# Kernel optimization log

Measured on AMD Instinct MI355X. Metric: run time of the kernel, lower is better.

## Reference

```python
import jax, jax.numpy as jnp
import numpy as np

B, Nq, Nk, R = 4, 1024, 1024, 256
NH, DK, DV = 8, 64, 64


def setup_inputs() -> dict:
    key = jax.random.key(0)
    ks = jax.random.split(key, 16)
    mk = lambda k, shape, s=1.0: jax.random.normal(k, shape, dtype=jnp.float32) * s
    inp = {
        'Q_real': mk(ks[0], (B, Nq, R)), 'Q_imag': mk(ks[1], (B, Nq, R)),
        'K_real': mk(ks[2], (B, Nk, R)), 'K_imag': mk(ks[3], (B, Nk, R)),
        'V_real': mk(ks[4], (B, Nk, R)), 'V_imag': mk(ks[5], (B, Nk, R)),
        'WQ_r': mk(ks[6], (NH * DK, R), 0.02), 'WQ_i': mk(ks[7], (NH * DK, R), 0.02),
        'WK_r': mk(ks[8], (NH * DK, R), 0.02), 'WK_i': mk(ks[9], (NH * DK, R), 0.02),
        'WV_r': mk(ks[10], (NH * DV, R), 0.02), 'WV_i': mk(ks[11], (NH * DV, R), 0.02),
        'WO_r': mk(ks[12], (R, NH * DV), 0.02), 'WO_i': mk(ks[13], (R, NH * DV), 0.02),
        'mask': jax.random.randint(ks[14], (B, Nk), 0, 2).astype(bool),
    }
    return inp


def _complex_linear(x, w_r, w_i):
    # x: complex [..., in]; weights real [out, in]. Same math as 4 real matmuls.
    w = (w_r + 1j * w_i).astype(jnp.complex64)
    return x @ w.T


def reference(Q_real, Q_imag, K_real, K_imag, V_real, V_imag,
              WQ_r, WQ_i, WK_r, WK_i, WV_r, WV_i, WO_r, WO_i, mask):
    Q = (Q_real + 1j * Q_imag).astype(jnp.complex64)
    K = (K_real + 1j * K_imag).astype(jnp.complex64)
    V = (V_real + 1j * V_imag).astype(jnp.complex64)

    Qp = _complex_linear(Q, WQ_r, WQ_i).reshape(B, Nq, NH, DK).transpose(0, 2, 1, 3)
    Kp = _complex_linear(K, WK_r, WK_i).reshape(B, Nk, NH, DK).transpose(0, 2, 1, 3)
    Vp = _complex_linear(V, WV_r, WV_i).reshape(B, Nk, NH, DV).transpose(0, 2, 1, 3)

    # complex scores [B, NH, Nq, Nk]; conj on K matches torch .conj().transpose
    scores = jnp.einsum('bhqd,bhkd->bhqk', Qp, jnp.conj(Kp)) / jnp.sqrt(jnp.float32(DK))
    scores_abs = jnp.abs(scores)

    m = mask[:, None, None, :]                    # [B,1,1,Nk]
    valid = jnp.any(mask, axis=-1)[:, None, None, None]  # [B,1,1,1] valid query rows
    masked = jnp.where(m, scores_abs, -jnp.inf)
    # avoid all -inf rows feeding softmax (those rows are zeroed afterwards)
    safe = jnp.where(valid, masked, 0.0)
    w = jax.nn.softmax(safe, axis=-1)
    w = jnp.where(valid, w, 0.0)

    attn = jnp.einsum('bhqk,bhkd->bhqd', w.astype(Vp.dtype), Vp)
    attn = attn.transpose(0, 2, 1, 3).reshape(B, Nq, NH * DV)
    return _complex_linear(attn, WO_r, WO_i)
```

## Files before the change

kernel.cpp:

```cpp
#include <hip/hip_runtime.h>
#include <math.h>

#define NBATCH 4
#define NSEQ   1024
#define RD     256
#define NHEAD  8
#define HD     64
#define NHD    512

typedef __attribute__((ext_vector_type(8))) short  short8;
typedef __attribute__((ext_vector_type(4))) short  short4v;
typedef __attribute__((ext_vector_type(4))) float  float4v;

#define MFMA16(a,b,c) __builtin_amdgcn_mfma_f32_16x16x32_bf16(a,b,c,0,0,0)

typedef const void __attribute__((address_space(1)))* gas_t;
typedef void __attribute__((address_space(3)))* las_t;
#define GLOAD16(g, l) __builtin_amdgcn_global_load_lds((gas_t)(g), (las_t)(l), 16, 0, 0)

static __device__ __forceinline__ unsigned short f2b(float f) {
    union { float f; unsigned u; } x; x.f = f;
    unsigned r = x.u + 0x7fffu + ((x.u >> 16) & 1u);
    return (unsigned short)(r >> 16);
}
static __device__ __forceinline__ void st4(short* dst, float4v v) {
    short4v p;
    p[0] = (short)f2b(v[0]); p[1] = (short)f2b(v[1]);
    p[2] = (short)f2b(v[2]); p[3] = (short)f2b(v[3]);
    *(short4v*)dst = p;
}

struct ConvArgs { const float* src[15]; short* dst[15]; int n4[15]; };

__global__ __launch_bounds__(256) void convert_bf16(ConvArgs ca)
{
    const int a = blockIdx.y;
    if (a == 14) {
        if (blockIdx.x != 0) return;
        __shared__ int isByteLayout;
        const int t = threadIdx.x;
        if (t == 0) isByteLayout = 0;
        __syncthreads();
        const int* mi = (const int*)ca.src[14];
        #pragma unroll
        for (int j = 0; j < 4; j++) {
            int v = mi[t*4 + j];
            if (v & ~1) isByteLayout = 1;
        }
        __syncthreads();
        unsigned char* nm = (unsigned char*)ca.dst[14];
        const unsigned char* mb = (const unsigned char*)ca.src[14];
        if (isByteLayout) {
            #pragma unroll
            for (int j = 0; j < 16; j++) { int k = t*16 + j; nm[k] = mb[k] ? 1 : 0; }
        } else {
            #pragma unroll
            for (int j = 0; j < 16; j++) { int k = t*16 + j; nm[k] = mi[k] ? 1 : 0; }
        }
        return;
    }
    const float* __restrict__ s = ca.src[a];
    short* __restrict__ d = ca.dst[a];
    const int n4 = ca.n4[a];
    for (int i = blockIdx.x*256 + threadIdx.x; i < n4; i += gridDim.x*256) {
        float4v v = *(const float4v*)(s + (size_t)i*4);
        st4(d + (size_t)i*4, v);
    }
}

struct ProjArgs {
    const short* Xr[3]; const short* Xi[3];
    const short* Wr[3]; const short* Wi[3];
    short* Yr[3]; short* Yi[3];
};

__global__ __launch_bounds__(256) void cgemm_proj(ProjArgs pa)
{
    __shared__ short sX[2][128][64];
    __shared__ short sW[2][64][64];
    const int z = blockIdx.z;
    const short* __restrict__ X_r = pa.Xr[z];
    const short* __restrict__ X_i = pa.Xi[z];
    const short* __restrict__ W_r = pa.Wr[z];
    const short* __restrict__ W_i = pa.Wi[z];
    short* __restrict__ Y_r = pa.Yr[z];
    short* __restrict__ Y_i = pa.Yi[z];
    const int transposeOut = (z == 2);

    const int tid  = threadIdx.x;
    const int lane = tid & 63, wave = tid >> 6;
    const int quad = lane >> 4, l16 = lane & 15;
    const int sw8  = l16 & 7;
    const int rsub = lane >> 3;
    const int colg = (lane & 7) ^ rsub;
    const int n0 = blockIdx.x * 64, m0 = blockIdx.y * 128;

    const short nk = (short)0x8000;
    const short8 neg = {nk,nk,nk,nk,nk,nk,nk,nk};

    float4v zf = {0.f,0.f,0.f,0.f};
    float4v Yr[2][4], Yi[2][4];
    #pragma unroll
    for (int ms = 0; ms < 2; ms++)
        #pragma unroll
        for (int t = 0; t < 4; t++) { Yr[ms][t] = zf; Yi[ms][t] = zf; }

    for (int kc = 0; kc < RD; kc += 64) {
        __syncthreads();
        if (wave < 2) {
            const short* gp = wave ? X_i : X_r;
            short* lp = wave ? &sX[1][0][0] : &sX[0][0][0];
            #pragma unroll
            for (int j = 0; j < 16; j++) {
                int row = j*8 + rsub;
                GLOAD16(gp + (size_t)(m0 + row)*RD + kc + colg*8, lp + j*512);
            }
        } else {
            const short* gp = (wave == 3) ? W_i : W_r;
            short* lp = (wave == 3) ? &sW[1][0][0] : &sW[0][0][0];
            #pragma unroll
            for (int j = 0; j < 8; j++) {
                int row = j*8 + rsub;
                GLOAD16(gp + (size_t)(n0 + row)*RD + kc + colg*8, lp + j*512);
            }
        }
        __syncthreads();
        short8 fxr[2][2], fxi[2][2], fxin[2][2];
        #pragma unroll
        for (int ms = 0; ms < 2; ms++)
            #pragma unroll
            for (int ds = 0; ds < 2; ds++) {
                int row = wave*32 + ms*16 + l16;
                int u = ((ds*4 + quad) ^ sw8) * 8;
                fxr[ms][ds]  = *(short8*)&sX[0][row][u];
                fxi[ms][ds]  = *(short8*)&sX[1][row][u];
                fxin[ms][ds] = fxi[ms][ds] ^ neg;
            }
        #pragma unroll
        for (int t = 0; t < 4; t++)
            #pragma unroll
            for (int ds = 0; ds < 2; ds++) {
                int u = ((ds*4 + quad) ^ sw8) * 8;
                short8 wr = *(short8*)&sW[0][t*16 + l16][u];
                short8 wi = *(short8*)&sW[1][t*16 + l16][u];
                #pragma unroll
                for (int ms = 0; ms < 2; ms++) {
                    Yr[ms][t] = MFMA16(fxr[ms][ds],  wr, Yr[ms][t]);
                    Yr[ms][t] = MFMA16(fxin[ms][ds], wi, Yr[ms][t]);
                    Yi[ms][t] = MFMA16(fxr[ms][ds],  wi, Yi[ms][t]);
                    Yi[ms][t] = MFMA16(fxi[ms][ds],  wr, Yi[ms][t]);
                }
            }
    }

    const int b = m0 >> 10, h = n0 >> 6, nb = m0 & 1023;
    short* sT = &sX[0][0][0];
    short* Yp[2] = { Y_r, Y_i };
    #pragma unroll
    for (int p = 0; p < 2; p++) {
        __syncthreads();
        #pragma unroll
        for (int ms = 0; ms < 2; ms++)
            #pragma unroll
            for (int t = 0; t < 4; t++)
                #pragma unroll
                for (int r = 0; r < 4; r++) {
                    float v = p ? Yi[ms][t][r] : Yr[ms][t][r];
                    int rr = wave*32 + ms*16 + quad*4 + r;
                    int cc = t*16 + l16;
                    if (!transposeOut) sT[rr*68 + cc]  = (short)f2b(v);
                    else               sT[cc*132 + rr] = (short)f2b(v);
                }
        __syncthreads();
        #pragma unroll
        for (int it = 0; it < 4; it++) {
            int idx = it*256 + tid;
            int rr, c8;
            size_t o;
            const short* sp;
            if (!transposeOut) {
                rr = idx >> 3; c8 = (idx & 7)*8;
                sp = &sT[rr*68 + c8];
                o = (((size_t)(b*NHEAD + h))*NSEQ + nb + rr)*HD + c8;
            } else {
                rr = idx >> 4; c8 = (idx & 15)*8;
                sp = &sT[rr*132 + c8];
                o = (((size_t)(b*NHEAD + h))*HD + rr)*NSEQ + nb + c8;
            }
            short4v a = *(short4v*)sp;
            short4v bq = *(short4v*)(sp + 4);
            short8 v8 = { a[0],a[1],a[2],a[3], bq[0],bq[1],bq[2],bq[3] };
            *(short8*)&Yp[p][o] = v8;
        }
    }
}

__global__ __launch_bounds__(512) void attn_mfma(
    const short* __restrict__ Qp_r, const short* __restrict__ Qp_i,
    const short* __restrict__ Kp_r, const short* __restrict__ Kp_i,
    const short* __restrict__ Vp_r, const short* __restrict__ Vp_i,
    const unsigned char* __restrict__ mask,
    short* __restrict__ Ar, short* __restrict__ Ai)
{
    __shared__ __align__(16) char smem[76800];
    short (*sP)[16][40] = (short(*)[16][40])(smem + 65536);
    unsigned char* smask = (unsigned char*)(smem + 75776);

    const int tid  = threadIdx.x;
    const int lane = tid & 63, wave = tid >> 6;
    const int quad = lane >> 4, l16 = lane & 15;
    const int sw8  = l16 & 7;
    const int qstrip = wave >> 1;
    const int khalf  = wave & 1;
    const int qt = blockIdx.x >> 5;
    const int bh = blockIdx.x & 31;
    const int b  = bh >> 3, h = bh & 7;
    const size_t base = (size_t)bh * (NSEQ*HD);

    const int rsub = lane >> 3;
    const int colg = (lane & 7) ^ rsub;

    if (tid < 256) ((int*)smask)[tid] = ((const int*)(mask + b*NSEQ))[tid];

    const int splane = wave >> 1;
    const short* sgp = (splane == 0) ? Kp_r : (splane == 1) ? Kp_i
                     : (splane == 2) ? Vp_r : Vp_i;
    const int sisV = (splane >= 2);
    const int soff = splane * 8192;

    const short nk = (short)0x8000;
    const short8 neg = {nk,nk,nk,nk,nk,nk,nk,nk};
    short8 fqr[2], fqi[2], fqrn[2];
    #pragma unroll
    for (int ds = 0; ds < 2; ds++) {
        size_t qo = base + (size_t)(qt*64 + qstrip*16 + l16)*HD + ds*32 + quad*8;
        fqr[ds]  = *(const short8*)&Qp_r[qo];
        fqi[ds]  = *(const short8*)&Qp_i[qo];
        fqrn[ds] = fqr[ds] ^ neg;
    }

    float4v zf = {0.f,0.f,0.f,0.f};
    float4v Or[4], Oi[4];
    float lrow[4];
    #pragma unroll
    for (int t = 0; t < 4; t++) { Or[t] = zf; Oi[t] = zf; }
    #pragma unroll
    for (int r = 0; r < 4; r++) lrow[r] = 0.f;

    const float C2 = 0.18033688f;

    {
        short* lp = (short*)(smem + soff);
        #pragma unroll
        for (int jj = 0; jj < 4; jj++) {
            int j = (wave & 1)*4 + jj;
            int row = j*8 + rsub;
            const short* g = sisV
                ? sgp + base + (size_t)row*NSEQ + colg*8
                : sgp + base + (size_t)row*HD + colg*8;
            GLOAD16(g, lp + j*512);
        }
    }

    for (int kt = 0; kt < 16; kt++) {
        __syncthreads();

        if (kt + 1 < 16) {
            const int kn = (kt + 1) * 64;
            short* lp = (short*)(smem + ((kt + 1) & 1)*32768 + soff);
            #pragma unroll
            for (int jj = 0; jj < 4; jj++) {
                int j = (wave & 1)*4 + jj;
                int row = j*8 + rsub;
                const short* g = sisV
                    ? sgp + base + (size_t)row*NSEQ + kn + colg*8
                    : sgp + base + (size_t)(kn + row)*HD + colg*8;
                GLOAD16(g, lp + j*512);
            }
        }

        const char* buf = smem + (kt & 1)*32768;
        short (*sK0)[64] = (short(*)[64])(buf);
        short (*sK1)[64] = (short(*)[64])(buf + 8192);
        short (*sV0)[64] = (short(*)[64])(buf + 16384);
        short (*sV1)[64] = (short(*)[64])(buf + 24576);
        const int k0 = kt*64;

        float4v Sr[2], Si[2];
        Sr[0] = zf; Sr[1] = zf; Si[0] = zf; Si[1] = zf;
        #pragma unroll
        for (int t = 0; t < 2; t++)
            #pragma unroll
            for (int ds = 0; ds < 2; ds++) {
                int u = ((ds*4 + quad) ^ sw8) * 8;
                int krow = khalf*32 + t*16 + l16;
                short8 kr = *(short8*)&sK0[krow][u];
                short8 ki = *(short8*)&sK1[krow][u];
                Sr[t] = MFMA16(fqr[ds],  kr, Sr[t]);
                Sr[t] = MFMA16(fqi[ds],  ki, Sr[t]);
                Si[t] = MFMA16(fqi[ds],  kr, Si[t]);
                Si[t] = MFMA16(fqrn[ds], ki, Si[t]);
            }

        #pragma unroll
        for (int t = 0; t < 2; t++) {
            bool mv = smask[k0 + khalf*32 + t*16 + l16] != 0;
            #pragma unroll
            for (int r = 0; r < 4; r++) {
                float a = Sr[t][r], c = Si[t][r];
                float x = fmaf(a, a, c*c);
                float s = __builtin_amdgcn_sqrtf(x);
                float e = mv ? __builtin_amdgcn_exp2f(C2 * s) : 0.f;
                lrow[r] += e;
                sP[wave][quad*4 + r][t*16 + l16] = (short)f2b(e);
            }
        }

        {
            short8 fp = *(short8*)&sP[wave][l16][quad*8];
            #pragma unroll
            for (int t = 0; t < 4; t++) {
                int u = ((khalf*4 + quad) ^ sw8) * 8;
                short8 vr = *(short8*)&sV0[t*16 + l16][u];
                short8 vi = *(short8*)&sV1[t*16 + l16][u];
                Or[t] = MFMA16(fp, vr, Or[t]);
                Oi[t] = MFMA16(fp, vi, Oi[t]);
            }
        }
    }

    __syncthreads();
    float* sC = (float*)smem;
    float* sL = (float*)(smem + 32768);
    if (khalf == 1) {
        #pragma unroll
        for (int t = 0; t < 4; t++)
            #pragma unroll
            for (int r = 0; r < 4; r++) {
                int o8 = ((qstrip*4 + t)*64 + lane)*8 + r*2;
                sC[o8]     = Or[t][r];
                sC[o8 + 1] = Oi[t][r];
            }
        int lo = (qstrip*64 + lane)*4;
        #pragma unroll
        for (int r = 0; r < 4; r++) sL[lo + r] = lrow[r];
    }
    __syncthreads();
    if (khalf == 0) {
        #pragma unroll
        for (int t = 0; t < 4; t++)
            #pragma unroll
            for (int r = 0; r < 4; r++) {
                int o8 = ((qstrip*4 + t)*64 + lane)*8 + r*2;
                Or[t][r] += sC[o8];
                Oi[t][r] += sC[o8 + 1];
            }
        int lo = (qstrip*64 + lane)*4;
        float inv[4];
        #pragma unroll
        for (int r = 0; r < 4; r++) {
            float ls = lrow[r] + sL[lo + r];
            ls += __shfl_xor(ls, 1, 64);
            ls += __shfl_xor(ls, 2, 64);
            ls += __shfl_xor(ls, 4, 64);
            ls += __shfl_xor(ls, 8, 64);
            inv[r] = (ls > 0.f) ? 1.f/ls : 0.f;
        }
        #pragma unroll
        for (int t = 0; t < 4; t++)
            #pragma unroll
            for (int r = 0; r < 4; r++) {
                int q = qt*64 + qstrip*16 + quad*4 + r;
                int d = t*16 + l16;
                size_t o = ((size_t)(b*NSEQ + q))*NHD + h*HD + d;
                Ar[o] = (short)f2b(Or[t][r] * inv[r]);
                Ai[o] = (short)f2b(Oi[t][r] * inv[r]);
            }
    }
}

__global__ __launch_bounds__(256) void cgemm_out(
    const short* __restrict__ A_r, const short* __restrict__ A_i,
    const short* __restrict__ W_r, const short* __restrict__ W_i,
    float* __restrict__ Out, int writeImagPlane)
{
    __shared__ short sA[2][64][64];
    __shared__ short sW[2][32][64];
    const int tid  = threadIdx.x;
    const int lane = tid & 63, wave = tid >> 6;
    const int quad = lane >> 4, l16 = lane & 15;
    const int sw8  = l16 & 7;
    const int rsub = lane >> 3;
    const int colg = (lane & 7) ^ rsub;
    const int n0 = blockIdx.x * 32, m0 = blockIdx.y * 64;

    const short nk = (short)0x8000;
    const short8 neg = {nk,nk,nk,nk,nk,nk,nk,nk};

    float4v zf = {0.f,0.f,0.f,0.f};
    float4v Yr[2], Yi[2];
    #pragma unroll
    for (int t = 0; t < 2; t++) { Yr[t] = zf; Yi[t] = zf; }

    for (int kc = 0; kc < NHD; kc += 64) {
        __syncthreads();
        {
            if (wave < 2) {
                const short* gp = wave ? A_i : A_r;
                short* lp = wave ? &sA[1][0][0] : &sA[0][0][0];
                #pragma unroll
                for (int j = 0; j < 8; j++) {
                    int row = j*8 + rsub;
                    GLOAD16(gp + (size_t)(m0 + row)*NHD + kc + colg*8, lp + j*512);
                }
            } else {
                const short* gp = (wave == 3) ? W_i : W_r;
                short* lp = (wave == 3) ? &sW[1][0][0] : &sW[0][0][0];
                #pragma unroll
                for (int j = 0; j < 4; j++) {
                    int row = j*8 + rsub;
                    GLOAD16(gp + (size_t)(n0 + row)*NHD + kc + colg*8, lp + j*512);
                }
            }
        }
        __syncthreads();
        short8 far[2], fai[2], fain[2];
        #pragma unroll
        for (int ds = 0; ds < 2; ds++) {
            int u = ((ds*4 + quad) ^ sw8) * 8;
            far[ds]  = *(short8*)&sA[0][wave*16 + l16][u];
            fai[ds]  = *(short8*)&sA[1][wave*16 + l16][u];
            fain[ds] = fai[ds] ^ neg;
        }
        #pragma unroll
        for (int t = 0; t < 2; t++)
            #pragma unroll
            for (int ds = 0; ds < 2; ds++) {
                int u = ((ds*4 + quad) ^ sw8) * 8;
                short8 wr = *(short8*)&sW[0][t*16 + l16][u];
                short8 wi = *(short8*)&sW[1][t*16 + l16][u];
                Yr[t] = MFMA16(far[ds],  wr, Yr[t]);
                Yr[t] = MFMA16(fain[ds], wi, Yr[t]);
                Yi[t] = MFMA16(far[ds],  wi, Yi[t]);
                Yi[t] = MFMA16(fai[ds],  wr, Yi[t]);
            }
    }
    const size_t TOT = (size_t)NBATCH * NSEQ * RD;
    #pragma unroll
    for (int t = 0; t < 2; t++)
        #pragma unroll
        for (int r = 0; r < 4; r++) {
            int row = m0 + wave*16 + quad*4 + r;
            int col = n0 + t*16 + l16;
            size_t o = (size_t)row*RD + col;
            Out[o] = Yr[t][r];
            if (writeImagPlane) Out[o + TOT] = Yi[t][r];
        }
}

extern "C" void kernel_launch(void* const* d_in, const int* in_sizes, int n_in,
                              void* d_out, int out_size, void* d_ws, size_t ws_size,
                              hipStream_t stream)
{
    float* out = (float*)d_out;

    const size_t P = (size_t)NBATCH * NHEAD * NSEQ * HD;
    const size_t H = (size_t)NBATCH * NSEQ * RD;
    const size_t WSZ = (size_t)NHD * RD;

    short* bws = (short*)d_ws;
    short* Qpr = bws + 0*P;  short* Qpi = bws + 1*P;
    short* Kpr = bws + 2*P;  short* Kpi = bws + 3*P;
    short* Vpr = bws + 4*P;  short* Vpi = bws + 5*P;
    short* conv = bws + 6*P;
    short* cX[6]; for (int i = 0; i < 6; i++) cX[i] = conv + i*H;
    short* cW[6]; for (int i = 0; i < 6; i++) cW[i] = conv + 6*H + i*WSZ;
    short* cWOr = conv + 6*H + 6*WSZ;
    short* cWOi = conv + 6*H + 7*WSZ;
    short* Apr = conv;
    short* Api = conv + P;
    unsigned char* nmask = (unsigned char*)(conv + 6*H + 8*WSZ);

    const size_t TOT = (size_t)NBATCH * NSEQ * RD;
    const int writeImagPlane = ((size_t)out_size >= 2*TOT) ? 1 : 0;

    ConvArgs ca;
    for (int i = 0; i < 6; i++) {
        ca.src[i] = (const float*)d_in[i];  ca.dst[i] = cX[i];  ca.n4[i] = (int)(H/4);
    }
    for (int i = 0; i < 6; i++) {
        ca.src[6+i] = (const float*)d_in[6+i]; ca.dst[6+i] = cW[i]; ca.n4[6+i] = (int)(WSZ/4);
    }
    ca.src[12] = (const float*)d_in[12]; ca.dst[12] = cWOr; ca.n4[12] = (int)(WSZ/4);
    ca.src[13] = (const float*)d_in[13]; ca.dst[13] = cWOi; ca.n4[13] = (int)(WSZ/4);
    ca.src[14] = (const float*)d_in[14]; ca.dst[14] = (short*)nmask; ca.n4[14] = 0;

    ProjArgs pa;
    pa.Xr[0] = cX[0]; pa.Xi[0] = cX[1];
    pa.Xr[1] = cX[2]; pa.Xi[1] = cX[3];
    pa.Xr[2] = cX[4]; pa.Xi[2] = cX[5];
    pa.Wr[0] = cW[0]; pa.Wi[0] = cW[1];
    pa.Wr[1] = cW[2]; pa.Wi[1] = cW[3];
    pa.Wr[2] = cW[4]; pa.Wi[2] = cW[5];
    pa.Yr[0] = Qpr; pa.Yi[0] = Qpi;
    pa.Yr[1] = Kpr; pa.Yi[1] = Kpi;
    pa.Yr[2] = Vpr; pa.Yi[2] = Vpi;

    convert_bf16<<<dim3(256, 15), 256, 0, stream>>>(ca);
    cgemm_proj<<<dim3(8, 32, 3), 256, 0, stream>>>(pa);
    attn_mfma<<<dim3(512), 512, 0, stream>>>(Qpr, Qpi, Kpr, Kpi, Vpr, Vpi,
                                             nmask, Apr, Api);
    cgemm_out<<<dim3(8, 64), 256, 0, stream>>>(Apr, Api, cWOr, cWOi, out,
                                               writeImagPlane);
}
```

Measured before the change: 172.7 us.

## Compact unmasked key/value rows before projection and attention to skip masked keys

The mask kernel now prefix-sums each batch's mask into a compacted index list and a count. A new gather kernel packs only the valid K and V rows, zero-padded to a multiple of 64. The K/V projection blocks past the padded count exit early, and the attention loop runs only over the valid key tiles, so masked keys cost no projection, MFMA or exp work. It adds one extra launch and a gather copy, and since the random mask keeps about half the keys, roughly half the K/V and attention work is removed.

```diff
diff --git a/kernel.cpp b/kernel.cpp
--- a/kernel.cpp
+++ b/kernel.cpp
@@ -48,15 +48,31 @@
             if (v & ~1) isByteLayout = 1;
         }
         __syncthreads();
-        unsigned char* nm = (unsigned char*)ca.dst[14];
         const unsigned char* mb = (const unsigned char*)ca.src[14];
+        unsigned char mv[16];
+        int lc = 0;
         if (isByteLayout) {
             #pragma unroll
-            for (int j = 0; j < 16; j++) { int k = t*16 + j; nm[k] = mb[k] ? 1 : 0; }
+            for (int j = 0; j < 16; j++) { mv[j] = mb[t*16 + j] ? 1 : 0; lc += mv[j]; }
         } else {
             #pragma unroll
-            for (int j = 0; j < 16; j++) { int k = t*16 + j; nm[k] = mi[k] ? 1 : 0; }
-        }
+            for (int j = 0; j < 16; j++) { mv[j] = mi[t*16 + j] ? 1 : 0; lc += mv[j]; }
+        }
+        const int lane = t & 63, b = t >> 6;
+        int sum = lc;
+        #pragma unroll
+        for (int d = 1; d < 64; d <<= 1) {
+            int o = __shfl_up(sum, d, 64);
+            if (lane >= d) sum += o;
+        }
+        int p = sum - lc;
+        unsigned short* idxOut = (unsigned short*)ca.dst[14];
+        int* cntOut = (int*)(idxOut + 4096);
+        unsigned short* ib = idxOut + b*1024;
+        #pragma unroll
+        for (int j = 0; j < 16; j++)
+            if (mv[j]) ib[p++] = (unsigned short)(lane*16 + j);
+        if (lane == 63) cntOut[b] = sum;
         return;
     }
     const float* __restrict__ s = ca.src[a];
@@ -68,10 +84,43 @@
     }
 }
 
+struct GatherArgs {
+    const short* src[4]; short* dst[4];
+    const unsigned short* idx; const int* cnt;
+};
+
+__global__ __launch_bounds__(256) void gather_rows(GatherArgs ga)
+{
+    const int p = blockIdx.z, b = blockIdx.y, ch = blockIdx.x;
+    const int tid = threadIdx.x;
+    const int cb = ga.cnt[b];
+    const int L  = (cb + 63) & ~63;
+    const short* s = ga.src[p] + (size_t)b*NSEQ*RD;
+    short* d       = ga.dst[p] + (size_t)b*NSEQ*RD;
+    const unsigned short* ib = ga.idx + b*1024;
+    #pragma unroll
+    for (int g = 0; g < 2; g++) {
+        int j = ch*64 + g*32 + (tid >> 3);
+        if (j >= L) continue;
+        short* dp = d + (size_t)j*RD + (tid & 7)*8;
+        if (j < cb) {
+            const short* sp = s + (size_t)ib[j]*RD + (tid & 7)*8;
+            #pragma unroll
+            for (int c = 0; c < 4; c++)
+                *(short8*)(dp + c*64) = *(const short8*)(sp + c*64);
+        } else {
+            short8 z = {0,0,0,0,0,0,0,0};
+            #pragma unroll
+            for (int c = 0; c < 4; c++) *(short8*)(dp + c*64) = z;
+        }
+    }
+}
+
 struct ProjArgs {
     const short* Xr[3]; const short* Xi[3];
     const short* Wr[3]; const short* Wi[3];
     short* Yr[3]; short* Yi[3];
+    const int* cnt;
 };
 
 __global__ __launch_bounds__(256) void cgemm_proj(ProjArgs pa)
@@ -79,6 +128,13 @@
     __shared__ short sX[2][128][64];
     __shared__ short sW[2][64][64];
     const int z = blockIdx.z;
+    const int n0 = blockIdx.x * 64, m0 = blockIdx.y * 128;
+    if (z >= 1) {
+        int b  = m0 >> 10;
+        int nb = m0 & 1023;
+        int L  = (pa.cnt[b] + 63) & ~63;
+        if (nb >= L) return;
+    }
     const short* __restrict__ X_r = pa.Xr[z];
     const short* __restrict__ X_i = pa.Xi[z];
     const short* __restrict__ W_r = pa.Wr[z];
@@ -93,7 +149,6 @@
     const int sw8  = l16 & 7;
     const int rsub = lane >> 3;
     const int colg = (lane & 7) ^ rsub;
-    const int n0 = blockIdx.x * 64, m0 = blockIdx.y * 128;
 
     const short nk = (short)0x8000;
     const short8 neg = {nk,nk,nk,nk,nk,nk,nk,nk};
@@ -199,12 +254,11 @@
     const short* __restrict__ Qp_r, const short* __restrict__ Qp_i,
     const short* __restrict__ Kp_r, const short* __restrict__ Kp_i,
     const short* __restrict__ Vp_r, const short* __restrict__ Vp_i,
-    const unsigned char* __restrict__ mask,
+    const int* __restrict__ cnt,
     short* __restrict__ Ar, short* __restrict__ Ai)
 {
-    __shared__ __align__(16) char smem[76800];
+    __shared__ __align__(16) char smem[75776];
     short (*sP)[16][40] = (short(*)[16][40])(smem + 65536);
-    unsigned char* smask = (unsigned char*)(smem + 75776);
 
     const int tid  = threadIdx.x;
     const int lane = tid & 63, wave = tid >> 6;
@@ -220,7 +274,8 @@
     const int rsub = lane >> 3;
     const int colg = (lane & 7) ^ rsub;
 
-    if (tid < 256) ((int*)smask)[tid] = ((const int*)(mask + b*NSEQ))[tid];
+    const int cb = cnt[b];
+    const int nt = (cb + 63) >> 6;
 
     const int splane = wave >> 1;
     const short* sgp = (splane == 0) ? Kp_r : (splane == 1) ? Kp_i
@@ -249,7 +304,7 @@
 
     const float C2 = 0.18033688f;
 
-    {
+    if (nt > 0) {
         short* lp = (short*)(smem + soff);
         #pragma unroll
         for (int jj = 0; jj < 4; jj++) {
@@ -262,10 +317,10 @@
         }
     }
 
-    for (int kt = 0; kt < 16; kt++) {
-        __syncthreads();
-
-        if (kt + 1 < 16) {
+    for (int kt = 0; kt < nt; kt++) {
+        __syncthreads();
+
+        if (kt + 1 < nt) {
             const int kn = (kt + 1) * 64;
             short* lp = (short*)(smem + ((kt + 1) & 1)*32768 + soff);
             #pragma unroll
@@ -304,7 +359,7 @@
 
         #pragma unroll
         for (int t = 0; t < 2; t++) {
-            bool mv = smask[k0 + khalf*32 + t*16 + l16] != 0;
+            bool mv = (k0 + khalf*32 + t*16 + l16) < cb;
             #pragma unroll
             for (int r = 0; r < 4; r++) {
                 float a = Sr[t][r], c = Si[t][r];
@@ -477,9 +532,13 @@
     short* cW[6]; for (int i = 0; i < 6; i++) cW[i] = conv + 6*H + i*WSZ;
     short* cWOr = conv + 6*H + 6*WSZ;
     short* cWOi = conv + 6*H + 7*WSZ;
+    short* gbuf = conv + 6*H + 8*WSZ;
+    short* gKr = gbuf + 0*H; short* gKi = gbuf + 1*H;
+    short* gVr = gbuf + 2*H; short* gVi = gbuf + 3*H;
+    unsigned short* midx = (unsigned short*)(gbuf + 4*H);
+    int* mcnt = (int*)(midx + 4096);
     short* Apr = conv;
     short* Api = conv + P;
-    unsigned char* nmask = (unsigned char*)(conv + 6*H + 8*WSZ);
 
     const size_t TOT = (size_t)NBATCH * NSEQ * RD;
     const int writeImagPlane = ((size_t)out_size >= 2*TOT) ? 1 : 0;
@@ -493,23 +552,30 @@
     }
     ca.src[12] = (const float*)d_in[12]; ca.dst[12] = cWOr; ca.n4[12] = (int)(WSZ/4);
     ca.src[13] = (const float*)d_in[13]; ca.dst[13] = cWOi; ca.n4[13] = (int)(WSZ/4);
-    ca.src[14] = (const float*)d_in[14]; ca.dst[14] = (short*)nmask; ca.n4[14] = 0;
+    ca.src[14] = (const float*)d_in[14]; ca.dst[14] = (short*)midx; ca.n4[14] = 0;
+
+    GatherArgs ga;
+    ga.src[0] = cX[2]; ga.src[1] = cX[3]; ga.src[2] = cX[4]; ga.src[3] = cX[5];
+    ga.dst[0] = gKr;   ga.dst[1] = gKi;   ga.dst[2] = gVr;   ga.dst[3] = gVi;
+    ga.idx = midx; ga.cnt = mcnt;
 
     ProjArgs pa;
     pa.Xr[0] = cX[0]; pa.Xi[0] = cX[1];
-    pa.Xr[1] = cX[2]; pa.Xi[1] = cX[3];
-    pa.Xr[2] = cX[4]; pa.Xi[2] = cX[5];
+    pa.Xr[1] = gKr;   pa.Xi[1] = gKi;
+    pa.Xr[2] = gVr;   pa.Xi[2] = gVi;
     pa.Wr[0] = cW[0]; pa.Wi[0] = cW[1];
     pa.Wr[1] = cW[2]; pa.Wi[1] = cW[3];
     pa.Wr[2] = cW[4]; pa.Wi[2] = cW[5];
     pa.Yr[0] = Qpr; pa.Yi[0] = Qpi;
     pa.Yr[1] = Kpr; pa.Yi[1] = Kpi;
     pa.Yr[2] = Vpr; pa.Yi[2] = Vpi;
+    pa.cnt = mcnt;
 
     convert_bf16<<<dim3(256, 15), 256, 0, stream>>>(ca);
+    gather_rows<<<dim3(16, 4, 4), 256, 0, stream>>>(ga);
     cgemm_proj<<<dim3(8, 32, 3), 256, 0, stream>>>(pa);
     attn_mfma<<<dim3(512), 512, 0, stream>>>(Qpr, Qpi, Kpr, Kpi, Vpr, Vpi,
-                                             nmask, Apr, Api);
+                                             mcnt, Apr, Api);
     cgemm_out<<<dim3(8, 64), 256, 0, stream>>>(Apr, Api, cWOr, cWOi, out,
                                                writeImagPlane);
 }
```

Result: faster. 164.1 us (-5.0%).
